# Kernel tuning notes

Hardware: AMD Instinct MI355X
Metric: run time of the kernel (lower is better)

The kernel has to match this reference:

```python
import jax, jax.numpy as jnp
import numpy as np

N = 1500                 # number of proposals
NUM_CLASSES = 81         # COCO: background + 80
NMS_THRESH = 0.5
SCORE_THRESH = 0.05
MAX_DET = 100            # config.test.max_det
BBOX_REG_WEIGHTS = jnp.array([10.0, 10.0, 5.0, 5.0], dtype=jnp.float32)


def setup_inputs() -> dict:
    key = jax.random.key(0)
    k1, k2, k3 = jax.random.split(key, 3)
    H, W = 800.0, 1333.0
    # realistic proposals: random centers / sizes inside the image
    cx = jax.random.uniform(jax.random.fold_in(k1, 0), (N,)) * W
    cy = jax.random.uniform(jax.random.fold_in(k1, 1), (N,)) * H
    bw = jax.random.uniform(jax.random.fold_in(k1, 2), (N,)) * 200.0 + 16.0
    bh = jax.random.uniform(jax.random.fold_in(k1, 3), (N,)) * 200.0 + 16.0
    bottom_rois = jnp.stack(
        [jnp.zeros((N,)), cx - 0.5 * bw, cy - 0.5 * bh, cx + 0.5 * bw, cy + 0.5 * bh],
        axis=1).astype(jnp.float32)
    bbox_delta = (jax.random.normal(k2, (N, 4 * NUM_CLASSES)) * 0.5).astype(jnp.float32)
    cls_prob = jax.nn.softmax(jax.random.normal(k3, (N, NUM_CLASSES)) * 2.0, axis=-1).astype(jnp.float32)
    im_info = jnp.array([[H, W, 1.0]], dtype=jnp.float32)
    return {"bottom_rois": bottom_rois, "bbox_delta": bbox_delta,
            "cls_prob": cls_prob, "im_info": im_info}


def _decode_boxes(rois, deltas, im_info):
    # rois [N,4], deltas [N,4C] -> clipped boxes [N,C,4] (legacy +1 convention)
    x1, y1, x2, y2 = rois[:, 0], rois[:, 1], rois[:, 2], rois[:, 3]
    w = x2 - x1 + 1.0
    h = y2 - y1 + 1.0
    cx = x1 + 0.5 * w
    cy = y1 + 0.5 * h
    d = deltas.reshape(deltas.shape[0], -1, 4) / BBOX_REG_WEIGHTS  # [N,C,4]
    pcx = cx[:, None] + w[:, None] * d[..., 0]
    pcy = cy[:, None] + h[:, None] * d[..., 1]
    pw = w[:, None] * jnp.exp(d[..., 2])
    ph = h[:, None] * jnp.exp(d[..., 3])
    boxes = jnp.stack([pcx - 0.5 * pw, pcy - 0.5 * ph,
                       pcx + 0.5 * pw - 1.0, pcy + 0.5 * ph - 1.0], axis=-1)
    hw = im_info[0, :2]  # [height, width]
    lim = jnp.stack([hw[1] - 1.0, hw[0] - 1.0, hw[1] - 1.0, hw[0] - 1.0])
    return jnp.clip(boxes, 0.0, lim)


def _pairwise_iou(b):
    # b [N,4], legacy +1 areas (matches gpu_nms)
    x1, y1, x2, y2 = b[:, 0], b[:, 1], b[:, 2], b[:, 3]
    area = (x2 - x1 + 1.0) * (y2 - y1 + 1.0)
    iw = jnp.maximum(jnp.minimum(x2[:, None], x2[None, :]) - jnp.maximum(x1[:, None], x1[None, :]) + 1.0, 0.0)
    ih = jnp.maximum(jnp.minimum(y2[:, None], y2[None, :]) - jnp.maximum(y1[:, None], y1[None, :]) + 1.0, 0.0)
    inter = iw * ih
    return inter / (area[:, None] + area[None, :] - inter)


def _nms_one_class(boxes, scores):
    # boxes [N,4], scores [N] -> score-sorted boxes/scores + keep mask
    valid = scores > SCORE_THRESH
    order = jnp.argsort(-scores)
    b = boxes[order]
    s = scores[order]
    v = valid[order]
    iou = jax.lax.stop_gradient(_pairwise_iou(b))  # used only in comparisons

    def body(suppressed, i):
        keep_i = v[i] & ~suppressed[i]
        suppressed = suppressed | (keep_i & (iou[i] > NMS_THRESH))
        return suppressed, keep_i

    _, keep = jax.lax.scan(body, jnp.zeros((b.shape[0],), bool), jnp.arange(b.shape[0]))
    return b, s, keep


def reference(bottom_rois, bbox_delta, cls_prob, im_info):
    boxes = _decode_boxes(bottom_rois[:, 1:], bbox_delta, im_info)  # [N,C,4]
    C = cls_prob.shape[1]
    boxes_fg = jnp.swapaxes(boxes, 0, 1)[1:]   # [C-1,N,4]
    scores_fg = cls_prob.T[1:]                 # [C-1,N]
    b, s, keep = jax.vmap(_nms_one_class)(boxes_fg, scores_fg)
    # image-level max_det cap (>= kth score, as in source)
    flat = jnp.where(keep, s, -jnp.inf).reshape(-1)
    n_keep = keep.sum()
    kth = jax.lax.top_k(flat, MAX_DET)[0][-1]
    keep = keep & jnp.where(n_keep > MAX_DET, s >= kth, True)
    cls_idx = jnp.broadcast_to(jnp.arange(1, C)[:, None], s.shape)
    zeros = jnp.zeros_like(s[..., None])
    dets = jnp.concatenate([zeros, b, s[..., None]], axis=-1)  # [C-1,N,6]
    dets = jnp.where(keep[..., None], dets, 0.0).reshape(-1, 6)
    return dets, cls_idx.reshape(-1), keep.reshape(-1)
```

## Files before the change

### kernel.cpp

```cpp
#include <hip/hip_runtime.h>
#include <math.h>

#pragma clang fp contract(off)

#define N_ROIS     1500
#define NUM_CLS    81
#define FG         80
#define MAXC       1536
#define NMS_T      0.5f
#define SCORE_T    0.05f
#define MAX_DET    100
#define TOTAL      (FG * N_ROIS)
#define TPB        256
#define NCHUNK     ((N_ROIS + TPB - 1) / TPB)
#define SUBCAP     8192

__device__ __forceinline__ unsigned f2s(float f) {
    unsigned u = __float_as_uint(f);
    return (u & 0x80000000u) ? ~u : (u | 0x80000000u);
}
__device__ __forceinline__ float s2f(unsigned u) {
    return __uint_as_float((u & 0x80000000u) ? (u & 0x7FFFFFFFu) : ~u);
}

__global__ __launch_bounds__(TPB) void nms_k1(
    const float* __restrict__ rois,
    const float* __restrict__ deltas,
    const float* __restrict__ prob,
    const float* __restrict__ iminfo,
    float4* __restrict__ keptBox,
    int*    __restrict__ keptRow,
    float*  __restrict__ keptScore,
    int*    __restrict__ ctrs)
{
    __shared__ unsigned long long key[MAXC];
    __shared__ unsigned long long skey[MAXC];
    __shared__ float4 box4[MAXC];
    __shared__ float  areaA[MAXC];
    __shared__ unsigned char keepf[MAXC], supp[MAXC];
    __shared__ int mcnt;

    const int tid  = threadIdx.x;
    const int lane = tid & 63;
    const int wv   = tid >> 6;
    const int c = blockIdx.x + 1;
    const int cbase = blockIdx.x * N_ROIS;

    if (tid == 0) mcnt = 0;
    __syncthreads();

    float sv[NCHUNK];
    #pragma unroll
    for (int t = 0; t < NCHUNK; ++t) {
        int i = t * TPB + tid;
        sv[t] = (i < N_ROIS) ? prob[i * NUM_CLS + c] : 0.0f;
    }
    #pragma unroll
    for (int t = 0; t < NCHUNK; ++t) {
        int i = t * TPB + tid;
        bool val = (i < N_ROIS) && (sv[t] > SCORE_T);
        unsigned long long m = __ballot(val);
        int base = 0;
        if (lane == 0 && m) base = atomicAdd(&mcnt, __popcll(m));
        base = __shfl(base, 0, 64);
        if (val) {
            int pos = base + __popcll(m & ((1ull << lane) - 1ull));
            key[pos] = ((unsigned long long)(~f2s(sv[t])) << 32) | (unsigned)i;
        }
    }
    __syncthreads();
    const int M = mcnt;
    if (M == 0) return;

    for (int i = tid; i < M; i += TPB) {
        unsigned long long kk = key[i];
        int cnt = 0;
        #pragma unroll 4
        for (int j = 0; j < M; ++j) cnt += (int)(key[j] < kk);
        skey[cnt] = kk;
    }
    __syncthreads();

    const float Hm1 = iminfo[0] - 1.0f;
    const float Wm1 = iminfo[1] - 1.0f;
    for (int k = tid; k < M; k += TPB) {
        unsigned long long kk = skey[k];
        int i = (int)(kk & 0xFFFFFFFFu);
        const float* rp = rois + i * 5;
        float x1 = rp[1], y1 = rp[2], x2 = rp[3], y2 = rp[4];
        float w  = x2 - x1 + 1.0f;
        float h  = y2 - y1 + 1.0f;
        float cx = x1 + 0.5f * w;
        float cy = y1 + 0.5f * h;
        const float* dp = deltas + i * (4 * NUM_CLS) + c * 4;
        float dx = dp[0] / 10.0f, dy = dp[1] / 10.0f;
        float dw = dp[2] / 5.0f,  dh = dp[3] / 5.0f;
        float pcx = cx + w * dx;
        float pcy = cy + h * dy;
        float pw  = w * expf(dw);
        float ph  = h * expf(dh);
        float a1 = pcx - 0.5f * pw;
        float a2 = pcy - 0.5f * ph;
        float a3 = pcx + 0.5f * pw - 1.0f;
        float a4 = pcy + 0.5f * ph - 1.0f;
        a1 = fminf(fmaxf(a1, 0.0f), Wm1);
        a2 = fminf(fmaxf(a2, 0.0f), Hm1);
        a3 = fminf(fmaxf(a3, 0.0f), Wm1);
        a4 = fminf(fmaxf(a4, 0.0f), Hm1);
        box4[k]  = make_float4(a1, a2, a3, a4);
        areaA[k] = (a3 - a1 + 1.0f) * (a4 - a2 + 1.0f);
        keepf[k] = 0; supp[k] = 0;
    }
    __syncthreads();

    const int MW = (M + 63) >> 6;
    const bool fast = (M * MW <= MAXC);

    if (fast) {
        for (int r = wv; r < M; r += TPB / 64) {
            float4 br = box4[r];
            float  ar = areaA[r];
            const int w0 = r >> 6;
            if (lane == 0)
                for (int w = 0; w < w0; ++w) key[r * MW + w] = 0ull;
            for (int w = w0; w < MW; ++w) {
                int col = (w << 6) | lane;
                bool inb = (col < M);
                int j = inb ? col : 0;
                float4 bj = box4[j];
                float  aj = areaA[j];
                float iw = fminf(br.z, bj.z) - fmaxf(br.x, bj.x) + 1.0f;
                float ih = fminf(br.w, bj.w) - fmaxf(br.y, bj.y) + 1.0f;
                iw = fmaxf(iw, 0.0f);
                ih = fmaxf(ih, 0.0f);
                float inter = iw * ih;
                float iou = inter / ((ar + aj) - inter);
                bool pred = inb && (col > r) && (iou > NMS_T);
                unsigned long long mk = __ballot(pred);
                if (lane == 0) key[r * MW + w] = mk;
            }
        }
        __syncthreads();

        if (tid < 64) {
            const int lw = (tid < MW) ? tid : 0;
            unsigned long long acc = 0;
            unsigned long long mcur = key[lw];
            for (int k = 0; k < M; ++k) {
                unsigned long long mnext =
                    (k + 1 < M) ? key[(k + 1) * MW + lw] : 0ull;
                int bit = (int)((acc >> (k & 63)) & 1ull);
                int sup = __shfl(bit, k >> 6, 64);
                if (!sup) {
                    acc |= mcur;
                    if (tid == 0) keepf[k] = 1;
                }
                mcur = mnext;
            }
        }
        __syncthreads();
    } else {
        for (int k = 0; k < M; ++k) {
            if (!supp[k]) {
                if (tid == 0) keepf[k] = 1;
                float4 bk = box4[k];
                float  ak = areaA[k];
                for (int j = k + 1 + tid; j < M; j += TPB) {
                    float4 bj = box4[j];
                    float  aj = areaA[j];
                    float iw = fminf(bk.z, bj.z) - fmaxf(bk.x, bj.x) + 1.0f;
                    float ih = fminf(bk.w, bj.w) - fmaxf(bk.y, bj.y) + 1.0f;
                    iw = fmaxf(iw, 0.0f);
                    ih = fmaxf(ih, 0.0f);
                    float inter = iw * ih;
                    float iou = inter / ((ak + aj) - inter);
                    if (iou > NMS_T) supp[j] = 1;
                }
            }
            __syncthreads();
        }
    }

    for (int k = tid; k < M; k += TPB) {
        if (keepf[k]) {
            int p = atomicAdd(&ctrs[0], 1);
            keptRow[p]   = cbase + k;
            keptBox[p]   = box4[k];
            keptScore[p] = s2f(~(unsigned)(skey[k] >> 32));
        }
    }
}

__global__ __launch_bounds__(TPB) void kth_k2(
    const int*   __restrict__ ctrs,
    const float* __restrict__ keptScore,
    float* __restrict__ kth_out)
{
    __shared__ int hist4[4][256];
    __shared__ unsigned sub[SUBCAP];
    __shared__ int wtot[4];
    __shared__ unsigned s_d0;
    __shared__ unsigned s_sp;
    __shared__ int s_kk, s_cnt;

    const int tid  = threadIdx.x;
    const int lane = tid & 63;
    const int wv   = tid >> 6;
    const int n = ctrs[0];

    if (n <= MAX_DET) {
        if (tid == 0) *kth_out = -INFINITY;
        return;
    }

    #pragma unroll
    for (int w = 0; w < 4; ++w) hist4[w][tid] = 0;
    __syncthreads();
    for (int i = tid; i < n; i += TPB)
        atomicAdd(&hist4[wv][f2s(keptScore[i]) >> 24], 1);
    __syncthreads();
    {
        const int h = hist4[0][tid] + hist4[1][tid] + hist4[2][tid] + hist4[3][tid];
        int r = h;
        #pragma unroll
        for (int off = 1; off < 64; off <<= 1) {
            int o = __shfl_down(r, off, 64);
            if (lane + off < 64) r += o;
        }
        if (lane == 0) wtot[wv] = r;
        __syncthreads();
        int hi = 0;
        #pragma unroll
        for (int w2 = 0; w2 < 4; ++w2) if (w2 > wv) hi += wtot[w2];
        const int S_ge = r + hi, S_gt = S_ge - h;
        if (S_gt < MAX_DET && S_ge >= MAX_DET) {
            s_d0 = (unsigned)tid;
            s_kk = MAX_DET - S_gt;
        }
    }
    if (tid == 0) { s_cnt = 0; s_sp = 0u; }
    __syncthreads();
    const unsigned d0 = s_d0;

    for (int i0 = 0; i0 < n; i0 += TPB) {
        int i = i0 + tid;
        unsigned u = (i < n) ? f2s(keptScore[i]) : 0u;
        bool match = (i < n) && ((u >> 24) == d0);
        unsigned long long m = __ballot(match);
        int base = 0;
        if (lane == 0 && m) base = atomicAdd(&s_cnt, __popcll(m));
        base = __shfl(base, 0, 64);
        if (match) {
            int pos = base + __popcll(m & ((1ull << lane) - 1ull));
            if (pos < SUBCAP) sub[pos] = u & 0xFFFFFFu;
        }
    }
    __syncthreads();
    const int ns = s_cnt;
    const bool inLds = (ns <= SUBCAP);
    const int limit = inLds ? ns : n;

    for (int d = 1; d < 4; ++d) {
        const int shift = 24 - 8 * d;
        #pragma unroll
        for (int w = 0; w < 4; ++w) hist4[w][tid] = 0;
        __syncthreads();
        const unsigned sp = s_sp;
        for (int i = tid; i < limit; i += TPB) {
            unsigned v; bool ok;
            if (inLds) { v = sub[i]; ok = true; }
            else {
                unsigned u = f2s(keptScore[i]);
                ok = ((u >> 24) == d0);
                v = u & 0xFFFFFFu;
            }
            if (ok && (d == 1 || (v >> (shift + 8)) == sp))
                atomicAdd(&hist4[wv][(v >> shift) & 255u], 1);
        }
        __syncthreads();
        const int h = hist4[0][tid] + hist4[1][tid] + hist4[2][tid] + hist4[3][tid];
        int r = h;
        #pragma unroll
        for (int off = 1; off < 64; off <<= 1) {
            int o = __shfl_down(r, off, 64);
            if (lane + off < 64) r += o;
        }
        if (lane == 0) wtot[wv] = r;
        __syncthreads();
        int hi = 0;
        #pragma unroll
        for (int w2 = 0; w2 < 4; ++w2) if (w2 > wv) hi += wtot[w2];
        const int S_ge = r + hi, S_gt = S_ge - h;
        const int kk = s_kk;
        if (S_gt < kk && S_ge >= kk) {
            s_sp = (s_sp << 8) | (unsigned)tid;
            s_kk = kk - S_gt;
        }
        __syncthreads();
    }

    if (tid == 0) *kth_out = s2f((d0 << 24) | s_sp);
}

__global__ __launch_bounds__(TPB) void fill_k3(float* __restrict__ out)
{
    const float4 z4 = make_float4(0.f, 0.f, 0.f, 0.f);
    const int stride = gridDim.x * TPB;
    int g = blockIdx.x * TPB + threadIdx.x;

    float4* dets4 = (float4*)out;
    for (int i = g; i < TOTAL * 6 / 4; i += stride) dets4[i] = z4;

    float4* cls4  = (float4*)(out + (size_t)TOTAL * 6);
    float4* keep4 = (float4*)(out + (size_t)TOTAL * 7);
    for (int i = g; i < TOTAL / 4; i += stride) {
        float fc = (float)((i * 4) / N_ROIS + 1);
        cls4[i]  = make_float4(fc, fc, fc, fc);
        keep4[i] = z4;
    }
}

__global__ __launch_bounds__(TPB) void patch_k4(
    const int*    __restrict__ ctrs,
    const int*    __restrict__ keptRow,
    const float4* __restrict__ keptBox,
    const float*  __restrict__ keptScore,
    const float*  __restrict__ kth_ptr,
    float* __restrict__ out)
{
    const int n = ctrs[0];
    const float kth = *kth_ptr;
    const int stride = gridDim.x * TPB;
    for (int i = blockIdx.x * TPB + threadIdx.x; i < n; i += stride) {
        float s = keptScore[i];
        if (s >= kth) {
            int r = keptRow[i];
            float4 b4 = keptBox[i];
            float* dst = out + (size_t)r * 6;
            dst[1] = b4.x; dst[2] = b4.y; dst[3] = b4.z; dst[4] = b4.w; dst[5] = s;
            out[(size_t)TOTAL * 7 + r] = 1.0f;
        }
    }
}

extern "C" void kernel_launch(void* const* d_in, const int* in_sizes, int n_in,
                              void* d_out, int out_size, void* d_ws, size_t ws_size,
                              hipStream_t stream) {
    const float* rois   = (const float*)d_in[0];
    const float* deltas = (const float*)d_in[1];
    const float* prob   = (const float*)d_in[2];
    const float* iminfo = (const float*)d_in[3];
    float* out = (float*)d_out;

    float4* keptBox   = (float4*)d_ws;
    int*    keptRow   = (int*)(keptBox + TOTAL);
    float*  keptScore = (float*)(keptRow + TOTAL);
    int*    ctrs      = (int*)(keptScore + TOTAL);
    float*  kth       = (float*)(ctrs + 4);

    hipMemsetAsync(ctrs, 0, sizeof(int), stream);
    nms_k1<<<FG, TPB, 0, stream>>>(rois, deltas, prob, iminfo,
                                   keptBox, keptRow, keptScore, ctrs);
    kth_k2<<<1, TPB, 0, stream>>>(ctrs, keptScore, kth);
    fill_k3<<<256, TPB, 0, stream>>>(out);
    patch_k4<<<64, TPB, 0, stream>>>(ctrs, keptRow, keptBox, keptScore, kth, out);
}
```

Measured before the change: 109.5 us.

## Fuse NMS, kth-select, fill and patch into one cooperative kernel

Merges the four kernels into a single cooperative launch of 256 blocks. The first 80 blocks run per-class NMS while the remaining blocks zero-fill and write the output at the same time. Grid syncs then order the single-block kth-score selection and the final patch pass. This removes three kernel launches and the inter-kernel gaps, and overlaps the fill with NMS. The cost is two grid-wide barriers, plus shared memory aliased across phases to fit within one block's LDS budget.

New measurement: 176.7 us. +61.3%, slower.

```diff
diff --git a/kernel.cpp b/kernel.cpp
--- a/kernel.cpp
+++ b/kernel.cpp
@@ -1,7 +1,10 @@
 #include <hip/hip_runtime.h>
+#include <hip/hip_cooperative_groups.h>
 #include <math.h>
 
 #pragma clang fp contract(off)
+
+namespace cg = cooperative_groups;
 
 #define N_ROIS     1500
 #define NUM_CLS    81
@@ -12,6 +15,7 @@
 #define MAX_DET    100
 #define TOTAL      (FG * N_ROIS)
 #define TPB        256
+#define NBLK       256
 #define NCHUNK     ((N_ROIS + TPB - 1) / TPB)
 #define SUBCAP     8192
 
@@ -23,7 +27,7 @@
     return __uint_as_float((u & 0x80000000u) ? (u & 0x7FFFFFFFu) : ~u);
 }
 
-__global__ __launch_bounds__(TPB) void nms_k1(
+__global__ __launch_bounds__(TPB) void fused_all(
     const float* __restrict__ rois,
     const float* __restrict__ deltas,
     const float* __restrict__ prob,
@@ -31,314 +35,310 @@
     float4* __restrict__ keptBox,
     int*    __restrict__ keptRow,
     float*  __restrict__ keptScore,
-    int*    __restrict__ ctrs)
+    int*    __restrict__ ctrs,
+    float*  __restrict__ g_kth,
+    float*  __restrict__ out)
 {
-    __shared__ unsigned long long key[MAXC];
-    __shared__ unsigned long long skey[MAXC];
-    __shared__ float4 box4[MAXC];
-    __shared__ float  areaA[MAXC];
-    __shared__ unsigned char keepf[MAXC], supp[MAXC];
+    cg::grid_group grid = cg::this_grid();
+
+    __shared__ __align__(16) unsigned char smem[58368];
+    unsigned long long* key  = (unsigned long long*)(smem);
+    unsigned long long* skey = (unsigned long long*)(smem + 12288);
+    float4* box4  = (float4*)(smem + 24576);
+    float*  areaA = (float*) (smem + 49152);
+    unsigned char* keepf = smem + 55296;
+    unsigned char* supp  = smem + 56832;
+    int (*hist4)[256] = (int(*)[256])(smem);
+    unsigned* sub = (unsigned*)(smem + 4096);
     __shared__ int mcnt;
+    __shared__ int wtot[4];
+    __shared__ unsigned s_d0, s_sp;
+    __shared__ int s_kk, s_cnt;
 
     const int tid  = threadIdx.x;
     const int lane = tid & 63;
     const int wv   = tid >> 6;
-    const int c = blockIdx.x + 1;
-    const int cbase = blockIdx.x * N_ROIS;
-
-    if (tid == 0) mcnt = 0;
-    __syncthreads();
-
-    float sv[NCHUNK];
-    #pragma unroll
-    for (int t = 0; t < NCHUNK; ++t) {
-        int i = t * TPB + tid;
-        sv[t] = (i < N_ROIS) ? prob[i * NUM_CLS + c] : 0.0f;
+    const int b    = blockIdx.x;
+
+    if (b < FG) {
+        const int c = b + 1;
+        const int cbase = b * N_ROIS;
+
+        if (tid == 0) mcnt = 0;
+        __syncthreads();
+
+        float svv[NCHUNK];
+        #pragma unroll
+        for (int t = 0; t < NCHUNK; ++t) {
+            int i = t * TPB + tid;
+            svv[t] = (i < N_ROIS) ? prob[i * NUM_CLS + c] : 0.0f;
+        }
+        #pragma unroll
+        for (int t = 0; t < NCHUNK; ++t) {
+            int i = t * TPB + tid;
+            bool val = (i < N_ROIS) && (svv[t] > SCORE_T);
+            unsigned long long m = __ballot(val);
+            int base = 0;
+            if (lane == 0 && m) base = atomicAdd(&mcnt, __popcll(m));
+            base = __shfl(base, 0, 64);
+            if (val) {
+                int pos = base + __popcll(m & ((1ull << lane) - 1ull));
+                key[pos] = ((unsigned long long)(~f2s(svv[t])) << 32) | (unsigned)i;
+            }
+        }
+        __syncthreads();
+        const int M = mcnt;
+
+        if (M > 0) {
+            for (int i = tid; i < M; i += TPB) {
+                unsigned long long kk = key[i];
+                int cnt = 0;
+                #pragma unroll 4
+                for (int j = 0; j < M; ++j) cnt += (int)(key[j] < kk);
+                skey[cnt] = kk;
+            }
+            __syncthreads();
+
+            const float Hm1 = iminfo[0] - 1.0f;
+            const float Wm1 = iminfo[1] - 1.0f;
+            for (int k = tid; k < M; k += TPB) {
+                unsigned long long kk = skey[k];
+                int i = (int)(kk & 0xFFFFFFFFu);
+                const float* rp = rois + i * 5;
+                float x1 = rp[1], y1 = rp[2], x2 = rp[3], y2 = rp[4];
+                float w  = x2 - x1 + 1.0f;
+                float h  = y2 - y1 + 1.0f;
+                float cx = x1 + 0.5f * w;
+                float cy = y1 + 0.5f * h;
+                const float* dp = deltas + i * (4 * NUM_CLS) + c * 4;
+                float dx = dp[0] / 10.0f, dy = dp[1] / 10.0f;
+                float dw = dp[2] / 5.0f,  dh = dp[3] / 5.0f;
+                float pcx = cx + w * dx;
+                float pcy = cy + h * dy;
+                float pw  = w * expf(dw);
+                float ph  = h * expf(dh);
+                float a1 = pcx - 0.5f * pw;
+                float a2 = pcy - 0.5f * ph;
+                float a3 = pcx + 0.5f * pw - 1.0f;
+                float a4 = pcy + 0.5f * ph - 1.0f;
+                a1 = fminf(fmaxf(a1, 0.0f), Wm1);
+                a2 = fminf(fmaxf(a2, 0.0f), Hm1);
+                a3 = fminf(fmaxf(a3, 0.0f), Wm1);
+                a4 = fminf(fmaxf(a4, 0.0f), Hm1);
+                box4[k]  = make_float4(a1, a2, a3, a4);
+                areaA[k] = (a3 - a1 + 1.0f) * (a4 - a2 + 1.0f);
+                keepf[k] = 0; supp[k] = 0;
+            }
+            __syncthreads();
+
+            const int MW = (M + 63) >> 6;
+            const bool fastp = (M * MW <= MAXC);
+
+            if (fastp) {
+                for (int r = wv; r < M; r += TPB / 64) {
+                    float4 br = box4[r];
+                    float  ar = areaA[r];
+                    const int w0 = r >> 6;
+                    if (lane == 0)
+                        for (int w = 0; w < w0; ++w) key[r * MW + w] = 0ull;
+                    for (int w = w0; w < MW; ++w) {
+                        int col = (w << 6) | lane;
+                        bool inb = (col < M);
+                        int j = inb ? col : 0;
+                        float4 bj = box4[j];
+                        float  aj = areaA[j];
+                        float iw = fminf(br.z, bj.z) - fmaxf(br.x, bj.x) + 1.0f;
+                        float ih = fminf(br.w, bj.w) - fmaxf(br.y, bj.y) + 1.0f;
+                        iw = fmaxf(iw, 0.0f);
+                        ih = fmaxf(ih, 0.0f);
+                        float inter = iw * ih;
+                        float iou = inter / ((ar + aj) - inter);
+                        bool pred = inb && (col > r) && (iou > NMS_T);
+                        unsigned long long mk = __ballot(pred);
+                        if (lane == 0) key[r * MW + w] = mk;
+                    }
+                }
+                __syncthreads();
+
+                if (tid < 64) {
+                    const int lw = (tid < MW) ? tid : 0;
+                    unsigned long long acc = 0;
+                    unsigned long long mcur = key[lw];
+                    for (int k = 0; k < M; ++k) {
+                        unsigned long long mnext =
+                            (k + 1 < M) ? key[(k + 1) * MW + lw] : 0ull;
+                        int bit = (int)((acc >> (k & 63)) & 1ull);
+                        int sup = __shfl(bit, k >> 6, 64);
+                        if (!sup) {
+                            acc |= mcur;
+                            if (tid == 0) keepf[k] = 1;
+                        }
+                        mcur = mnext;
+                    }
+                }
+                __syncthreads();
+            } else {
+                for (int k = 0; k < M; ++k) {
+                    if (!supp[k]) {
+                        if (tid == 0) keepf[k] = 1;
+                        float4 bk = box4[k];
+                        float  ak = areaA[k];
+                        for (int j = k + 1 + tid; j < M; j += TPB) {
+                            float4 bj = box4[j];
+                            float  aj = areaA[j];
+                            float iw = fminf(bk.z, bj.z) - fmaxf(bk.x, bj.x) + 1.0f;
+                            float ih = fminf(bk.w, bj.w) - fmaxf(bk.y, bj.y) + 1.0f;
+                            iw = fmaxf(iw, 0.0f);
+                            ih = fmaxf(ih, 0.0f);
+                            float inter = iw * ih;
+                            float iou = inter / ((ak + aj) - inter);
+                            if (iou > NMS_T) supp[j] = 1;
+                        }
+                    }
+                    __syncthreads();
+                }
+            }
+
+            for (int k = tid; k < M; k += TPB) {
+                if (keepf[k]) {
+                    int p = atomicAdd(&ctrs[0], 1);
+                    keptRow[p]   = cbase + k;
+                    keptBox[p]   = box4[k];
+                    keptScore[p] = s2f(~(unsigned)(skey[k] >> 32));
+                }
+            }
+        }
+    } else {
+        const float4 z4 = make_float4(0.f, 0.f, 0.f, 0.f);
+        const int stride = (NBLK - FG) * TPB;
+        int g = (b - FG) * TPB + tid;
+
+        float4* dets4 = (float4*)out;
+        for (int i = g; i < TOTAL * 6 / 4; i += stride) dets4[i] = z4;
+
+        float4* cls4  = (float4*)(out + (size_t)TOTAL * 6);
+        float4* keep4 = (float4*)(out + (size_t)TOTAL * 7);
+        for (int i = g; i < TOTAL / 4; i += stride) {
+            float fc = (float)((i * 4) / N_ROIS + 1);
+            cls4[i]  = make_float4(fc, fc, fc, fc);
+            keep4[i] = z4;
+        }
     }
-    #pragma unroll
-    for (int t = 0; t < NCHUNK; ++t) {
-        int i = t * TPB + tid;
-        bool val = (i < N_ROIS) && (sv[t] > SCORE_T);
-        unsigned long long m = __ballot(val);
-        int base = 0;
-        if (lane == 0 && m) base = atomicAdd(&mcnt, __popcll(m));
-        base = __shfl(base, 0, 64);
-        if (val) {
-            int pos = base + __popcll(m & ((1ull << lane) - 1ull));
-            key[pos] = ((unsigned long long)(~f2s(sv[t])) << 32) | (unsigned)i;
+
+    grid.sync();
+
+    if (b == 0) {
+        const int n = ctrs[0];
+        if (n <= MAX_DET) {
+            if (tid == 0) *g_kth = -INFINITY;
+        } else {
+            #pragma unroll
+            for (int w = 0; w < 4; ++w) hist4[w][tid] = 0;
+            __syncthreads();
+            for (int i = tid; i < n; i += TPB)
+                atomicAdd(&hist4[wv][f2s(keptScore[i]) >> 24], 1);
+            __syncthreads();
+            {
+                const int h = hist4[0][tid] + hist4[1][tid] +
+                              hist4[2][tid] + hist4[3][tid];
+                int r = h;
+                #pragma unroll
+                for (int off = 1; off < 64; off <<= 1) {
+                    int o = __shfl_down(r, off, 64);
+                    if (lane + off < 64) r += o;
+                }
+                if (lane == 0) wtot[wv] = r;
+                __syncthreads();
+                int hi = 0;
+                #pragma unroll
+                for (int w2 = 0; w2 < 4; ++w2) if (w2 > wv) hi += wtot[w2];
+                const int S_ge = r + hi, S_gt = S_ge - h;
+                if (S_gt < MAX_DET && S_ge >= MAX_DET) {
+                    s_d0 = (unsigned)tid;
+                    s_kk = MAX_DET - S_gt;
+                }
+            }
+            if (tid == 0) { s_cnt = 0; s_sp = 0u; }
+            __syncthreads();
+            const unsigned d0 = s_d0;
+
+            for (int i0 = 0; i0 < n; i0 += TPB) {
+                int i = i0 + tid;
+                unsigned u = (i < n) ? f2s(keptScore[i]) : 0u;
+                bool match = (i < n) && ((u >> 24) == d0);
+                unsigned long long m = __ballot(match);
+                int base = 0;
+                if (lane == 0 && m) base = atomicAdd(&s_cnt, __popcll(m));
+                base = __shfl(base, 0, 64);
+                if (match) {
+                    int pos = base + __popcll(m & ((1ull << lane) - 1ull));
+                    if (pos < SUBCAP) sub[pos] = u & 0xFFFFFFu;
+                }
+            }
+            __syncthreads();
+            const int ns = s_cnt;
+            const bool inLds = (ns <= SUBCAP);
+            const int limit = inLds ? ns : n;
+
+            for (int d = 1; d < 4; ++d) {
+                const int shift = 24 - 8 * d;
+                #pragma unroll
+                for (int w = 0; w < 4; ++w) hist4[w][tid] = 0;
+                __syncthreads();
+                const unsigned sp = s_sp;
+                for (int i = tid; i < limit; i += TPB) {
+                    unsigned v; bool ok;
+                    if (inLds) { v = sub[i]; ok = true; }
+                    else {
+                        unsigned u = f2s(keptScore[i]);
+                        ok = ((u >> 24) == d0);
+                        v = u & 0xFFFFFFu;
+                    }
+                    if (ok && (d == 1 || (v >> (shift + 8)) == sp))
+                        atomicAdd(&hist4[wv][(v >> shift) & 255u], 1);
+                }
+                __syncthreads();
+                const int h = hist4[0][tid] + hist4[1][tid] +
+                              hist4[2][tid] + hist4[3][tid];
+                int r = h;
+                #pragma unroll
+                for (int off = 1; off < 64; off <<= 1) {
+                    int o = __shfl_down(r, off, 64);
+                    if (lane + off < 64) r += o;
+                }
+                if (lane == 0) wtot[wv] = r;
+                __syncthreads();
+                int hi = 0;
+                #pragma unroll
+                for (int w2 = 0; w2 < 4; ++w2) if (w2 > wv) hi += wtot[w2];
+                const int S_ge = r + hi, S_gt = S_ge - h;
+                const int kk = s_kk;
+                if (S_gt < kk && S_ge >= kk) {
+                    s_sp = (s_sp << 8) | (unsigned)tid;
+                    s_kk = kk - S_gt;
+                }
+                __syncthreads();
+            }
+            if (tid == 0) *g_kth = s2f((d0 << 24) | s_sp);
         }
     }
-    __syncthreads();
-    const int M = mcnt;
-    if (M == 0) return;
-
-    for (int i = tid; i < M; i += TPB) {
-        unsigned long long kk = key[i];
-        int cnt = 0;
-        #pragma unroll 4
-        for (int j = 0; j < M; ++j) cnt += (int)(key[j] < kk);
-        skey[cnt] = kk;
-    }
-    __syncthreads();
-
-    const float Hm1 = iminfo[0] - 1.0f;
-    const float Wm1 = iminfo[1] - 1.0f;
-    for (int k = tid; k < M; k += TPB) {
-        unsigned long long kk = skey[k];
-        int i = (int)(kk & 0xFFFFFFFFu);
-        const float* rp = rois + i * 5;
-        float x1 = rp[1], y1 = rp[2], x2 = rp[3], y2 = rp[4];
-        float w  = x2 - x1 + 1.0f;
-        float h  = y2 - y1 + 1.0f;
-        float cx = x1 + 0.5f * w;
-        float cy = y1 + 0.5f * h;
-        const float* dp = deltas + i * (4 * NUM_CLS) + c * 4;
-        float dx = dp[0] / 10.0f, dy = dp[1] / 10.0f;
-        float dw = dp[2] / 5.0f,  dh = dp[3] / 5.0f;
-        float pcx = cx + w * dx;
-        float pcy = cy + h * dy;
-        float pw  = w * expf(dw);
-        float ph  = h * expf(dh);
-        float a1 = pcx - 0.5f * pw;
-        float a2 = pcy - 0.5f * ph;
-        float a3 = pcx + 0.5f * pw - 1.0f;
-        float a4 = pcy + 0.5f * ph - 1.0f;
-        a1 = fminf(fmaxf(a1, 0.0f), Wm1);
-        a2 = fminf(fmaxf(a2, 0.0f), Hm1);
-        a3 = fminf(fmaxf(a3, 0.0f), Wm1);
-        a4 = fminf(fmaxf(a4, 0.0f), Hm1);
-        box4[k]  = make_float4(a1, a2, a3, a4);
-        areaA[k] = (a3 - a1 + 1.0f) * (a4 - a2 + 1.0f);
-        keepf[k] = 0; supp[k] = 0;
-    }
-    __syncthreads();
-
-    const int MW = (M + 63) >> 6;
-    const bool fast = (M * MW <= MAXC);
-
-    if (fast) {
-        for (int r = wv; r < M; r += TPB / 64) {
-            float4 br = box4[r];
-            float  ar = areaA[r];
-            const int w0 = r >> 6;
-            if (lane == 0)
-                for (int w = 0; w < w0; ++w) key[r * MW + w] = 0ull;
-            for (int w = w0; w < MW; ++w) {
-                int col = (w << 6) | lane;
-                bool inb = (col < M);
-                int j = inb ? col : 0;
-                float4 bj = box4[j];
-                float  aj = areaA[j];
-                float iw = fminf(br.z, bj.z) - fmaxf(br.x, bj.x) + 1.0f;
-                float ih = fminf(br.w, bj.w) - fmaxf(br.y, bj.y) + 1.0f;
-                iw = fmaxf(iw, 0.0f);
-                ih = fmaxf(ih, 0.0f);
-                float inter = iw * ih;
-                float iou = inter / ((ar + aj) - inter);
-                bool pred = inb && (col > r) && (iou > NMS_T);
-                unsigned long long mk = __ballot(pred);
-                if (lane == 0) key[r * MW + w] = mk;
-            }
-        }
-        __syncthreads();
-
-        if (tid < 64) {
-            const int lw = (tid < MW) ? tid : 0;
-            unsigned long long acc = 0;
-            unsigned long long mcur = key[lw];
-            for (int k = 0; k < M; ++k) {
-                unsigned long long mnext =
-                    (k + 1 < M) ? key[(k + 1) * MW + lw] : 0ull;
-                int bit = (int)((acc >> (k & 63)) & 1ull);
-                int sup = __shfl(bit, k >> 6, 64);
-                if (!sup) {
-                    acc |= mcur;
-                    if (tid == 0) keepf[k] = 1;
-                }
-                mcur = mnext;
-            }
-        }
-        __syncthreads();
-    } else {
-        for (int k = 0; k < M; ++k) {
-            if (!supp[k]) {
-                if (tid == 0) keepf[k] = 1;
-                float4 bk = box4[k];
-                float  ak = areaA[k];
-                for (int j = k + 1 + tid; j < M; j += TPB) {
-                    float4 bj = box4[j];
-                    float  aj = areaA[j];
-                    float iw = fminf(bk.z, bj.z) - fmaxf(bk.x, bj.x) + 1.0f;
-                    float ih = fminf(bk.w, bj.w) - fmaxf(bk.y, bj.y) + 1.0f;
-                    iw = fmaxf(iw, 0.0f);
-                    ih = fmaxf(ih, 0.0f);
-                    float inter = iw * ih;
-                    float iou = inter / ((ak + aj) - inter);
-                    if (iou > NMS_T) supp[j] = 1;
-                }
-            }
-            __syncthreads();
-        }
-    }
-
-    for (int k = tid; k < M; k += TPB) {
-        if (keepf[k]) {
-            int p = atomicAdd(&ctrs[0], 1);
-            keptRow[p]   = cbase + k;
-            keptBox[p]   = box4[k];
-            keptScore[p] = s2f(~(unsigned)(skey[k] >> 32));
-        }
-    }
-}
-
-__global__ __launch_bounds__(TPB) void kth_k2(
-    const int*   __restrict__ ctrs,
-    const float* __restrict__ keptScore,
-    float* __restrict__ kth_out)
-{
-    __shared__ int hist4[4][256];
-    __shared__ unsigned sub[SUBCAP];
-    __shared__ int wtot[4];
-    __shared__ unsigned s_d0;
-    __shared__ unsigned s_sp;
-    __shared__ int s_kk, s_cnt;
-
-    const int tid  = threadIdx.x;
-    const int lane = tid & 63;
-    const int wv   = tid >> 6;
-    const int n = ctrs[0];
-
-    if (n <= MAX_DET) {
-        if (tid == 0) *kth_out = -INFINITY;
-        return;
-    }
-
-    #pragma unroll
-    for (int w = 0; w < 4; ++w) hist4[w][tid] = 0;
-    __syncthreads();
-    for (int i = tid; i < n; i += TPB)
-        atomicAdd(&hist4[wv][f2s(keptScore[i]) >> 24], 1);
-    __syncthreads();
+
+    grid.sync();
+
     {
-        const int h = hist4[0][tid] + hist4[1][tid] + hist4[2][tid] + hist4[3][tid];
-        int r = h;
-        #pragma unroll
-        for (int off = 1; off < 64; off <<= 1) {
-            int o = __shfl_down(r, off, 64);
-            if (lane + off < 64) r += o;
-        }
-        if (lane == 0) wtot[wv] = r;
-        __syncthreads();
-        int hi = 0;
-        #pragma unroll
-        for (int w2 = 0; w2 < 4; ++w2) if (w2 > wv) hi += wtot[w2];
-        const int S_ge = r + hi, S_gt = S_ge - h;
-        if (S_gt < MAX_DET && S_ge >= MAX_DET) {
-            s_d0 = (unsigned)tid;
-            s_kk = MAX_DET - S_gt;
-        }
-    }
-    if (tid == 0) { s_cnt = 0; s_sp = 0u; }
-    __syncthreads();
-    const unsigned d0 = s_d0;
-
-    for (int i0 = 0; i0 < n; i0 += TPB) {
-        int i = i0 + tid;
-        unsigned u = (i < n) ? f2s(keptScore[i]) : 0u;
-        bool match = (i < n) && ((u >> 24) == d0);
-        unsigned long long m = __ballot(match);
-        int base = 0;
-        if (lane == 0 && m) base = atomicAdd(&s_cnt, __popcll(m));
-        base = __shfl(base, 0, 64);
-        if (match) {
-            int pos = base + __popcll(m & ((1ull << lane) - 1ull));
-            if (pos < SUBCAP) sub[pos] = u & 0xFFFFFFu;
-        }
-    }
-    __syncthreads();
-    const int ns = s_cnt;
-    const bool inLds = (ns <= SUBCAP);
-    const int limit = inLds ? ns : n;
-
-    for (int d = 1; d < 4; ++d) {
-        const int shift = 24 - 8 * d;
-        #pragma unroll
-        for (int w = 0; w < 4; ++w) hist4[w][tid] = 0;
-        __syncthreads();
-        const unsigned sp = s_sp;
-        for (int i = tid; i < limit; i += TPB) {
-            unsigned v; bool ok;
-            if (inLds) { v = sub[i]; ok = true; }
-            else {
-                unsigned u = f2s(keptScore[i]);
-                ok = ((u >> 24) == d0);
-                v = u & 0xFFFFFFu;
-            }
-            if (ok && (d == 1 || (v >> (shift + 8)) == sp))
-                atomicAdd(&hist4[wv][(v >> shift) & 255u], 1);
-        }
-        __syncthreads();
-        const int h = hist4[0][tid] + hist4[1][tid] + hist4[2][tid] + hist4[3][tid];
-        int r = h;
-        #pragma unroll
-        for (int off = 1; off < 64; off <<= 1) {
-            int o = __shfl_down(r, off, 64);
-            if (lane + off < 64) r += o;
-        }
-        if (lane == 0) wtot[wv] = r;
-        __syncthreads();
-        int hi = 0;
-        #pragma unroll
-        for (int w2 = 0; w2 < 4; ++w2) if (w2 > wv) hi += wtot[w2];
-        const int S_ge = r + hi, S_gt = S_ge - h;
-        const int kk = s_kk;
-        if (S_gt < kk && S_ge >= kk) {
-            s_sp = (s_sp << 8) | (unsigned)tid;
-            s_kk = kk - S_gt;
-        }
-        __syncthreads();
-    }
-
-    if (tid == 0) *kth_out = s2f((d0 << 24) | s_sp);
-}
-
-__global__ __launch_bounds__(TPB) void fill_k3(float* __restrict__ out)
-{
-    const float4 z4 = make_float4(0.f, 0.f, 0.f, 0.f);
-    const int stride = gridDim.x * TPB;
-    int g = blockIdx.x * TPB + threadIdx.x;
-
-    float4* dets4 = (float4*)out;
-    for (int i = g; i < TOTAL * 6 / 4; i += stride) dets4[i] = z4;
-
-    float4* cls4  = (float4*)(out + (size_t)TOTAL * 6);
-    float4* keep4 = (float4*)(out + (size_t)TOTAL * 7);
-    for (int i = g; i < TOTAL / 4; i += stride) {
-        float fc = (float)((i * 4) / N_ROIS + 1);
-        cls4[i]  = make_float4(fc, fc, fc, fc);
-        keep4[i] = z4;
-    }
-}
-
-__global__ __launch_bounds__(TPB) void patch_k4(
-    const int*    __restrict__ ctrs,
-    const int*    __restrict__ keptRow,
-    const float4* __restrict__ keptBox,
-    const float*  __restrict__ keptScore,
-    const float*  __restrict__ kth_ptr,
-    float* __restrict__ out)
-{
-    const int n = ctrs[0];
-    const float kth = *kth_ptr;
-    const int stride = gridDim.x * TPB;
-    for (int i = blockIdx.x * TPB + threadIdx.x; i < n; i += stride) {
-        float s = keptScore[i];
-        if (s >= kth) {
-            int r = keptRow[i];
-            float4 b4 = keptBox[i];
-            float* dst = out + (size_t)r * 6;
-            dst[1] = b4.x; dst[2] = b4.y; dst[3] = b4.z; dst[4] = b4.w; dst[5] = s;
-            out[(size_t)TOTAL * 7 + r] = 1.0f;
+        const int n = ctrs[0];
+        const float kth = *g_kth;
+        const int stride = NBLK * TPB;
+        for (int i = b * TPB + tid; i < n; i += stride) {
+            float s = keptScore[i];
+            if (s >= kth) {
+                int r = keptRow[i];
+                float4 b4 = keptBox[i];
+                float* dst = out + (size_t)r * 6;
+                dst[1] = b4.x; dst[2] = b4.y; dst[3] = b4.z;
+                dst[4] = b4.w; dst[5] = s;
+                out[(size_t)TOTAL * 7 + r] = 1.0f;
+            }
         }
     }
 }
@@ -356,12 +356,13 @@
     int*    keptRow   = (int*)(keptBox + TOTAL);
     float*  keptScore = (float*)(keptRow + TOTAL);
     int*    ctrs      = (int*)(keptScore + TOTAL);
-    float*  kth       = (float*)(ctrs + 4);
+    float*  g_kth     = (float*)(ctrs + 4);
 
     hipMemsetAsync(ctrs, 0, sizeof(int), stream);
-    nms_k1<<<FG, TPB, 0, stream>>>(rois, deltas, prob, iminfo,
-                                   keptBox, keptRow, keptScore, ctrs);
-    kth_k2<<<1, TPB, 0, stream>>>(ctrs, keptScore, kth);
-    fill_k3<<<256, TPB, 0, stream>>>(out);
-    patch_k4<<<64, TPB, 0, stream>>>(ctrs, keptRow, keptBox, keptScore, kth, out);
+
+    void* args[] = { (void*)&rois, (void*)&deltas, (void*)&prob, (void*)&iminfo,
+                     (void*)&keptBox, (void*)&keptRow, (void*)&keptScore,
+                     (void*)&ctrs, (void*)&g_kth, (void*)&out };
+    hipLaunchCooperativeKernel((void*)fused_all, dim3(NBLK), dim3(TPB),
+                               args, 0, stream);
 }
```

## Fold output fill into NMS kernel and merge kth selection with patch

Applied to the files above, without the earlier changes.

Output zero-fill and class-index writes now run on extra blocks of the NMS kernel, overlapping with the per-class NMS blocks instead of being a separate launch. The kth radix select and the patch step are merged into one 1024-thread single-block kernel, so four launches become two. This removes launch overhead and the serial gaps between small kernels. The trade-offs are a single block doing the patch scatter, and the fill blocks sharing the GPU with the NMS blocks.

Result: faster. 104.4 us (median of 2 runs) (-4.7%).

```diff
diff --git a/kernel.cpp b/kernel.cpp
--- a/kernel.cpp
+++ b/kernel.cpp
@@ -12,6 +12,8 @@
 #define MAX_DET    100
 #define TOTAL      (FG * N_ROIS)
 #define TPB        256
+#define K1_BLOCKS  256
+#define K2_TPB     1024
 #define NCHUNK     ((N_ROIS + TPB - 1) / TPB)
 #define SUBCAP     8192
 
@@ -31,8 +33,32 @@
     float4* __restrict__ keptBox,
     int*    __restrict__ keptRow,
     float*  __restrict__ keptScore,
-    int*    __restrict__ ctrs)
+    int*    __restrict__ ctrs,
+    float*  __restrict__ out)
 {
+    const int tid  = threadIdx.x;
+    const int lane = tid & 63;
+    const int wv   = tid >> 6;
+    const int b    = blockIdx.x;
+
+    if (b >= FG) {
+        const float4 z4 = make_float4(0.f, 0.f, 0.f, 0.f);
+        const int stride = (K1_BLOCKS - FG) * TPB;
+        int g = (b - FG) * TPB + tid;
+
+        float4* dets4 = (float4*)out;
+        for (int i = g; i < TOTAL * 6 / 4; i += stride) dets4[i] = z4;
+
+        float4* cls4  = (float4*)(out + (size_t)TOTAL * 6);
+        float4* keep4 = (float4*)(out + (size_t)TOTAL * 7);
+        for (int i = g; i < TOTAL / 4; i += stride) {
+            float fc = (float)((i * 4) / N_ROIS + 1);
+            cls4[i]  = make_float4(fc, fc, fc, fc);
+            keep4[i] = z4;
+        }
+        return;
+    }
+
     __shared__ unsigned long long key[MAXC];
     __shared__ unsigned long long skey[MAXC];
     __shared__ float4 box4[MAXC];
@@ -40,11 +66,8 @@
     __shared__ unsigned char keepf[MAXC], supp[MAXC];
     __shared__ int mcnt;
 
-    const int tid  = threadIdx.x;
-    const int lane = tid & 63;
-    const int wv   = tid >> 6;
-    const int c = blockIdx.x + 1;
-    const int cbase = blockIdx.x * N_ROIS;
+    const int c = b + 1;
+    const int cbase = b * N_ROIS;
 
     if (tid == 0) mcnt = 0;
     __syncthreads();
@@ -191,147 +214,148 @@
     }
 }
 
-__global__ __launch_bounds__(TPB) void kth_k2(
-    const int*   __restrict__ ctrs,
-    const float* __restrict__ keptScore,
-    float* __restrict__ kth_out)
+__global__ __launch_bounds__(K2_TPB) void kth_patch_k2(
+    const int*    __restrict__ ctrs,
+    const int*    __restrict__ keptRow,
+    const float4* __restrict__ keptBox,
+    const float*  __restrict__ keptScore,
+    float* __restrict__ out)
 {
     __shared__ int hist4[4][256];
     __shared__ unsigned sub[SUBCAP];
     __shared__ int wtot[4];
-    __shared__ unsigned s_d0;
-    __shared__ unsigned s_sp;
+    __shared__ unsigned s_d0, s_sp;
     __shared__ int s_kk, s_cnt;
+    __shared__ float s_kth;
 
     const int tid  = threadIdx.x;
     const int lane = tid & 63;
     const int wv   = tid >> 6;
+    const int hp   = wv & 3;
     const int n = ctrs[0];
 
-    if (n <= MAX_DET) {
-        if (tid == 0) *kth_out = -INFINITY;
-        return;
-    }
-
-    #pragma unroll
-    for (int w = 0; w < 4; ++w) hist4[w][tid] = 0;
-    __syncthreads();
-    for (int i = tid; i < n; i += TPB)
-        atomicAdd(&hist4[wv][f2s(keptScore[i]) >> 24], 1);
-    __syncthreads();
-    {
-        const int h = hist4[0][tid] + hist4[1][tid] + hist4[2][tid] + hist4[3][tid];
-        int r = h;
-        #pragma unroll
-        for (int off = 1; off < 64; off <<= 1) {
-            int o = __shfl_down(r, off, 64);
-            if (lane + off < 64) r += o;
-        }
-        if (lane == 0) wtot[wv] = r;
-        __syncthreads();
-        int hi = 0;
-        #pragma unroll
-        for (int w2 = 0; w2 < 4; ++w2) if (w2 > wv) hi += wtot[w2];
-        const int S_ge = r + hi, S_gt = S_ge - h;
-        if (S_gt < MAX_DET && S_ge >= MAX_DET) {
-            s_d0 = (unsigned)tid;
-            s_kk = MAX_DET - S_gt;
-        }
-    }
-    if (tid == 0) { s_cnt = 0; s_sp = 0u; }
-    __syncthreads();
-    const unsigned d0 = s_d0;
-
-    for (int i0 = 0; i0 < n; i0 += TPB) {
-        int i = i0 + tid;
-        unsigned u = (i < n) ? f2s(keptScore[i]) : 0u;
-        bool match = (i < n) && ((u >> 24) == d0);
-        unsigned long long m = __ballot(match);
-        int base = 0;
-        if (lane == 0 && m) base = atomicAdd(&s_cnt, __popcll(m));
-        base = __shfl(base, 0, 64);
-        if (match) {
-            int pos = base + __popcll(m & ((1ull << lane) - 1ull));
-            if (pos < SUBCAP) sub[pos] = u & 0xFFFFFFu;
-        }
-    }
-    __syncthreads();
-    const int ns = s_cnt;
-    const bool inLds = (ns <= SUBCAP);
-    const int limit = inLds ? ns : n;
-
-    for (int d = 1; d < 4; ++d) {
-        const int shift = 24 - 8 * d;
-        #pragma unroll
-        for (int w = 0; w < 4; ++w) hist4[w][tid] = 0;
-        __syncthreads();
-        const unsigned sp = s_sp;
-        for (int i = tid; i < limit; i += TPB) {
-            unsigned v; bool ok;
-            if (inLds) { v = sub[i]; ok = true; }
-            else {
-                unsigned u = f2s(keptScore[i]);
-                ok = ((u >> 24) == d0);
-                v = u & 0xFFFFFFu;
-            }
-            if (ok && (d == 1 || (v >> (shift + 8)) == sp))
-                atomicAdd(&hist4[wv][(v >> shift) & 255u], 1);
-        }
-        __syncthreads();
-        const int h = hist4[0][tid] + hist4[1][tid] + hist4[2][tid] + hist4[3][tid];
-        int r = h;
-        #pragma unroll
-        for (int off = 1; off < 64; off <<= 1) {
-            int o = __shfl_down(r, off, 64);
-            if (lane + off < 64) r += o;
-        }
-        if (lane == 0) wtot[wv] = r;
-        __syncthreads();
-        int hi = 0;
-        #pragma unroll
-        for (int w2 = 0; w2 < 4; ++w2) if (w2 > wv) hi += wtot[w2];
-        const int S_ge = r + hi, S_gt = S_ge - h;
-        const int kk = s_kk;
-        if (S_gt < kk && S_ge >= kk) {
-            s_sp = (s_sp << 8) | (unsigned)tid;
-            s_kk = kk - S_gt;
-        }
-        __syncthreads();
-    }
-
-    if (tid == 0) *kth_out = s2f((d0 << 24) | s_sp);
-}
-
-__global__ __launch_bounds__(TPB) void fill_k3(float* __restrict__ out)
-{
-    const float4 z4 = make_float4(0.f, 0.f, 0.f, 0.f);
-    const int stride = gridDim.x * TPB;
-    int g = blockIdx.x * TPB + threadIdx.x;
-
-    float4* dets4 = (float4*)out;
-    for (int i = g; i < TOTAL * 6 / 4; i += stride) dets4[i] = z4;
-
-    float4* cls4  = (float4*)(out + (size_t)TOTAL * 6);
-    float4* keep4 = (float4*)(out + (size_t)TOTAL * 7);
-    for (int i = g; i < TOTAL / 4; i += stride) {
-        float fc = (float)((i * 4) / N_ROIS + 1);
-        cls4[i]  = make_float4(fc, fc, fc, fc);
-        keep4[i] = z4;
-    }
-}
-
-__global__ __launch_bounds__(TPB) void patch_k4(
-    const int*    __restrict__ ctrs,
-    const int*    __restrict__ keptRow,
-    const float4* __restrict__ keptBox,
-    const float*  __restrict__ keptScore,
-    const float*  __restrict__ kth_ptr,
-    float* __restrict__ out)
-{
-    const int n = ctrs[0];
-    const float kth = *kth_ptr;
-    const int stride = gridDim.x * TPB;
-    for (int i = blockIdx.x * TPB + threadIdx.x; i < n; i += stride) {
+    if (n > MAX_DET) {
+        if (tid < 1024) {
+            #pragma unroll
+            for (int w = 0; w < 4; ++w) if (tid < 256) hist4[w][tid] = 0;
+        }
+        __syncthreads();
+        for (int i = tid; i < n; i += K2_TPB)
+            atomicAdd(&hist4[hp][f2s(keptScore[i]) >> 24], 1);
+        __syncthreads();
+        if (tid < 256) {
+            const int h = hist4[0][tid] + hist4[1][tid] +
+                          hist4[2][tid] + hist4[3][tid];
+            int r = h;
+            #pragma unroll
+            for (int off = 1; off < 64; off <<= 1) {
+                int o = __shfl_down(r, off, 64);
+                if (lane + off < 64) r += o;
+            }
+            if (lane == 0) wtot[wv] = r;
+        }
+        __syncthreads();
+        if (tid < 256) {
+            const int h = hist4[0][tid] + hist4[1][tid] +
+                          hist4[2][tid] + hist4[3][tid];
+            int r = h;
+            #pragma unroll
+            for (int off = 1; off < 64; off <<= 1) {
+                int o = __shfl_down(r, off, 64);
+                if (lane + off < 64) r += o;
+            }
+            int hi = 0;
+            #pragma unroll
+            for (int w2 = 0; w2 < 4; ++w2) if (w2 > wv) hi += wtot[w2];
+            const int S_ge = r + hi, S_gt = S_ge - h;
+            if (S_gt < MAX_DET && S_ge >= MAX_DET) {
+                s_d0 = (unsigned)tid;
+                s_kk = MAX_DET - S_gt;
+            }
+        }
+        if (tid == 0) { s_cnt = 0; s_sp = 0u; }
+        __syncthreads();
+        const unsigned d0 = s_d0;
+
+        for (int i0 = 0; i0 < n; i0 += K2_TPB) {
+            int i = i0 + tid;
+            unsigned u = (i < n) ? f2s(keptScore[i]) : 0u;
+            bool match = (i < n) && ((u >> 24) == d0);
+            unsigned long long m = __ballot(match);
+            int base = 0;
+            if (lane == 0 && m) base = atomicAdd(&s_cnt, __popcll(m));
+            base = __shfl(base, 0, 64);
+            if (match) {
+                int pos = base + __popcll(m & ((1ull << lane) - 1ull));
+                if (pos < SUBCAP) sub[pos] = u & 0xFFFFFFu;
+            }
+        }
+        __syncthreads();
+        const int ns = s_cnt;
+        const bool inLds = (ns <= SUBCAP);
+        const int limit = inLds ? ns : n;
+
+        for (int d = 1; d < 4; ++d) {
+            const int shift = 24 - 8 * d;
+            if (tid < 256) {
+                #pragma unroll
+                for (int w = 0; w < 4; ++w) hist4[w][tid] = 0;
+            }
+            __syncthreads();
+            const unsigned sp = s_sp;
+            for (int i = tid; i < limit; i += K2_TPB) {
+                unsigned v; bool ok;
+                if (inLds) { v = sub[i]; ok = true; }
+                else {
+                    unsigned u = f2s(keptScore[i]);
+                    ok = ((u >> 24) == d0);
+                    v = u & 0xFFFFFFu;
+                }
+                if (ok && (d == 1 || (v >> (shift + 8)) == sp))
+                    atomicAdd(&hist4[hp][(v >> shift) & 255u], 1);
+            }
+            __syncthreads();
+            if (tid < 256) {
+                const int h = hist4[0][tid] + hist4[1][tid] +
+                              hist4[2][tid] + hist4[3][tid];
+                int r = h;
+                #pragma unroll
+                for (int off = 1; off < 64; off <<= 1) {
+                    int o = __shfl_down(r, off, 64);
+                    if (lane + off < 64) r += o;
+                }
+                if (lane == 0) wtot[wv] = r;
+            }
+            __syncthreads();
+            if (tid < 256) {
+                const int h = hist4[0][tid] + hist4[1][tid] +
+                              hist4[2][tid] + hist4[3][tid];
+                int r = h;
+                #pragma unroll
+                for (int off = 1; off < 64; off <<= 1) {
+                    int o = __shfl_down(r, off, 64);
+                    if (lane + off < 64) r += o;
+                }
+                int hi = 0;
+                #pragma unroll
+                for (int w2 = 0; w2 < 4; ++w2) if (w2 > wv) hi += wtot[w2];
+                const int S_ge = r + hi, S_gt = S_ge - h;
+                const int kk = s_kk;
+                if (S_gt < kk && S_ge >= kk) {
+                    s_sp = (s_sp << 8) | (unsigned)tid;
+                    s_kk = kk - S_gt;
+                }
+            }
+            __syncthreads();
+        }
+        if (tid == 0) s_kth = s2f((s_d0 << 24) | s_sp);
+    } else {
+        if (tid == 0) s_kth = -INFINITY;
+    }
+    __syncthreads();
+    const float kth = s_kth;
+
+    for (int i = tid; i < n; i += K2_TPB) {
         float s = keptScore[i];
         if (s >= kth) {
             int r = keptRow[i];
@@ -356,12 +380,9 @@
     int*    keptRow   = (int*)(keptBox + TOTAL);
     float*  keptScore = (float*)(keptRow + TOTAL);
     int*    ctrs      = (int*)(keptScore + TOTAL);
-    float*  kth       = (float*)(ctrs + 4);
 
     hipMemsetAsync(ctrs, 0, sizeof(int), stream);
-    nms_k1<<<FG, TPB, 0, stream>>>(rois, deltas, prob, iminfo,
-                                   keptBox, keptRow, keptScore, ctrs);
-    kth_k2<<<1, TPB, 0, stream>>>(ctrs, keptScore, kth);
-    fill_k3<<<256, TPB, 0, stream>>>(out);
-    patch_k4<<<64, TPB, 0, stream>>>(ctrs, keptRow, keptBox, keptScore, kth, out);
-}
+    nms_k1<<<K1_BLOCKS, TPB, 0, stream>>>(rois, deltas, prob, iminfo,
+                                          keptBox, keptRow, keptScore, ctrs, out);
+    kth_patch_k2<<<1, K2_TPB, 0, stream>>>(ctrs, keptRow, keptBox, keptScore, out);
+}
```
